# Kernel tuning notes

Hardware: AMD Instinct MI355X
Metric: run time of the kernel (lower is better)

## Reference

```python
import jax, jax.numpy as jnp
import numpy as np

N = 50000; E = 800000; B = 500; L = 42
F_IN = 35; HEADS = 10; F_H = 35; F_G = 350
VOCAB = 26; EMB = 128; NF = 16; OUT_DIM = 128; K = 8
NEG_SLOPE = 0.2


def setup_inputs() -> dict:
    key = jax.random.key(0)
    ks = jax.random.split(key, 16)
    inp = {}
    inp['x'] = jax.random.normal(ks[0], (N, F_IN), jnp.float32)
    inp['edge_index'] = jax.random.randint(ks[1], (2, E), 0, N, dtype=jnp.int32)
    inp['batch'] = jnp.sort(jax.random.randint(ks[2], (N,), 0, B, dtype=jnp.int32))
    inp['target'] = jax.random.randint(ks[3], (B, L), 0, VOCAB, dtype=jnp.int32)
    # --- learned parameters ---
    inp['W_gat'] = jax.random.normal(ks[4], (F_IN, HEADS * F_H), jnp.float32) * 0.1
    inp['att_src'] = jax.random.normal(ks[5], (HEADS, F_H), jnp.float32) * 0.1
    inp['att_dst'] = jax.random.normal(ks[6], (HEADS, F_H), jnp.float32) * 0.1
    inp['b_gat'] = jnp.zeros((HEADS * F_H,), jnp.float32)
    inp['W_gcn'] = jax.random.normal(ks[7], (F_G, F_G), jnp.float32) * 0.05
    inp['b_gcn'] = jnp.zeros((F_G,), jnp.float32)
    inp['W_fcg1'] = jax.random.normal(ks[8], (2 * F_G, 1500), jnp.float32) * 0.03
    inp['b_fcg1'] = jnp.zeros((1500,), jnp.float32)
    inp['W_fcg2'] = jax.random.normal(ks[9], (1500, OUT_DIM), jnp.float32) * 0.03
    inp['b_fcg2'] = jnp.zeros((OUT_DIM,), jnp.float32)
    inp['emb_xt'] = jax.random.normal(ks[10], (VOCAB, EMB), jnp.float32) * 0.1
    inp['W_conv'] = jax.random.normal(ks[11], (NF, EMB, K), jnp.float32) * 0.05
    inp['b_conv'] = jnp.zeros((NF,), jnp.float32)
    inp['W_fcxt'] = jax.random.normal(ks[12], (NF * 35, OUT_DIM), jnp.float32) * 0.05
    inp['b_fcxt'] = jnp.zeros((OUT_DIM,), jnp.float32)
    inp['W_fc1'] = jax.random.normal(ks[13], (256, 512), jnp.float32) * 0.05
    inp['b_fc1'] = jnp.zeros((512,), jnp.float32)
    inp['W_out'] = jax.random.normal(ks[14], (512, 1), jnp.float32) * 0.05
    inp['b_out'] = jnp.zeros((1,), jnp.float32)
    return inp


def _add_self_loops(edge_index):
    loop = jnp.arange(N, dtype=edge_index.dtype)
    src = jnp.concatenate([edge_index[0], loop])
    dst = jnp.concatenate([edge_index[1], loop])
    return src, dst


def _gat_conv(x, src, dst, W, att_src, att_dst, b):
    # h: [N, H, C]
    h = (x @ W).reshape(N, HEADS, F_H)
    a_s = jnp.einsum('nhc,hc->nh', h, att_src)  # [N, H]
    a_d = jnp.einsum('nhc,hc->nh', h, att_dst)
    e = jax.nn.leaky_relu(a_s[src] + a_d[dst], NEG_SLOPE)  # [Etot, H]
    # segment softmax over incoming edges per destination node, per head
    m = jax.ops.segment_max(e, dst, num_segments=N)
    m = jnp.where(jnp.isfinite(m), m, 0.0)
    ex = jnp.exp(e - m[dst])
    den = jax.ops.segment_sum(ex, dst, num_segments=N)
    alpha = ex / (den[dst] + 1e-16)  # [Etot, H]
    out = jax.ops.segment_sum(h[src] * alpha[:, :, None], dst, num_segments=N)
    return out.reshape(N, HEADS * F_H) + b, alpha


def _gcn_conv(x, src, dst, W, b):
    deg = jax.ops.segment_sum(jnp.ones_like(dst, jnp.float32), dst, num_segments=N)
    dinv = jnp.where(deg > 0, deg ** -0.5, 0.0)
    norm = dinv[src] * dinv[dst]  # symmetric normalization
    h = x @ W
    return jax.ops.segment_sum(h[src] * norm[:, None], dst, num_segments=N) + b


def reference(x, edge_index, batch, target, W_gat, att_src, att_dst, b_gat,
              W_gcn, b_gcn, W_fcg1, b_fcg1, W_fcg2, b_fcg2, emb_xt,
              W_conv, b_conv, W_fcxt, b_fcxt, W_fc1, b_fc1, W_out, b_out):
    src, dst = _add_self_loops(edge_index)
    # --- graph branch ---
    xg, alpha = _gat_conv(x, src, dst, W_gat, att_src, att_dst, b_gat)
    xg = jax.nn.relu(xg)
    xg = jax.nn.relu(_gcn_conv(xg, src, dst, W_gcn, b_gcn))
    # global max + mean pool per graph
    gmax = jax.ops.segment_max(xg, batch, num_segments=B)
    gsum = jax.ops.segment_sum(xg, batch, num_segments=B)
    cnt = jax.ops.segment_sum(jnp.ones((N,), jnp.float32), batch, num_segments=B)
    gmean = gsum / jnp.maximum(cnt, 1.0)[:, None]
    xg = jnp.concatenate([gmax, gmean], axis=1)  # [B, 700]
    xg = jax.nn.relu(xg @ W_fcg1 + b_fcg1)
    xg = xg @ W_fcg2 + b_fcg2  # [B, 128] (dropout is identity in eval)
    # --- protein branch ---
    emb = emb_xt[target]                      # [B, L, 128]
    emb = jnp.transpose(emb, (0, 2, 1))       # [B, 128, L]
    conv = jax.lax.conv_general_dilated(
        emb, W_conv, window_strides=(1,), padding='VALID',
        dimension_numbers=('NCH', 'OIH', 'NCH'))  # [B, 16, 35]
    conv = conv + b_conv[None, :, None]
    xt = conv.reshape(B, NF * 35)
    xt = xt @ W_fcxt + b_fcxt                 # [B, 128]
    # --- fusion ---
    xc = jnp.concatenate([xg, xt], axis=1)    # [B, 256]
    xc = jax.nn.relu(xc @ W_fc1 + b_fc1)
    out = jax.nn.sigmoid(xc @ W_out + b_out)  # [B, 1]
    return out, alpha
```

## Files before the change

### kernel.cpp

```cpp
#include <hip/hip_runtime.h>
#include <math.h>

#define NN 50000
#define EE 800000
#define BB 500
#define LL 42
#define NHEAD 10
#define FH 35
#define FG 350
#define ETOT (EE + NN)
#define NCHUNK ((NN + 511) / 512)

#define KPAD 384
#define LDH2 352
#define MPAD 50048
#define MB2  512

typedef unsigned short ushort_t;
typedef __attribute__((ext_vector_type(8))) short short8v;
typedef __attribute__((ext_vector_type(4))) float float4v;

__device__ __forceinline__ float lrelu(float x) { return x > 0.f ? x : 0.2f * x; }

__device__ __forceinline__ ushort_t f2bf(float f) {
    unsigned int u = __float_as_uint(f);
    u += 0x7fffu + ((u >> 16) & 1u);
    return (ushort_t)(u >> 16);
}
__device__ __forceinline__ float bflo(unsigned u) { return __uint_as_float(u << 16); }
__device__ __forceinline__ float bfhi(unsigned u) { return __uint_as_float(u & 0xffff0000u); }
__device__ __forceinline__ unsigned packbf(float a, float b) {
    return (unsigned)f2bf(a) | ((unsigned)f2bf(b) << 16);
}

__device__ __forceinline__ void async_cp16(const void* g, void* l) {
    __builtin_amdgcn_global_load_lds((const __attribute__((address_space(1))) unsigned int*)g,
                                     (__attribute__((address_space(3))) unsigned int*)l, 16, 0, 0);
}

__global__ __launch_bounds__(256) void k_init(int* deg, int* cur) {
    int i = blockIdx.x * 256 + threadIdx.x;
    if (i < NN) { deg[i] = 1; cur[i] = 0; }
}

__global__ __launch_bounds__(256) void k_deg(const int* __restrict__ ei, int* deg) {
    int i = blockIdx.x * 256 + threadIdx.x;
    if (i < EE) atomicAdd(&deg[ei[EE + i]], 1);
}

__global__ __launch_bounds__(512) void k_scan1(const int* __restrict__ deg, int* part) {
    int i = blockIdx.x * 512 + threadIdx.x;
    int lane = threadIdx.x & 63, wv = threadIdx.x >> 6;
    int x = (i < NN) ? deg[i] : 0;
    #pragma unroll
    for (int d = 32; d; d >>= 1) x += __shfl_xor(x, d);
    __shared__ int wsum[8];
    if (lane == 0) wsum[wv] = x;
    __syncthreads();
    if (threadIdx.x == 0) {
        int s = 0;
        #pragma unroll
        for (int w = 0; w < 8; w++) s += wsum[w];
        part[blockIdx.x] = s;
    }
}

__global__ __launch_bounds__(64) void k_scan2(const int* __restrict__ part, int* pscan) {
    int l = threadIdx.x;
    int v0 = (l < NCHUNK) ? part[l] : 0;
    #pragma unroll
    for (int d = 1; d < 64; d <<= 1) { int t = __shfl_up(v0, d); if (l >= d) v0 += t; }
    int tot0 = __shfl(v0, 63);
    int v1 = (64 + l < NCHUNK) ? part[64 + l] : 0;
    #pragma unroll
    for (int d = 1; d < 64; d <<= 1) { int t = __shfl_up(v1, d); if (l >= d) v1 += t; }
    v1 += tot0;
    if (l < NCHUNK) pscan[l] = v0;
    if (64 + l < NCHUNK) pscan[64 + l] = v1;
}

__global__ __launch_bounds__(512) void k_scan3(const int* __restrict__ deg, const int* __restrict__ pscan,
                                               int* offs) {
    int i = blockIdx.x * 512 + threadIdx.x;
    int lane = threadIdx.x & 63, wv = threadIdx.x >> 6;
    int x = (i < NN) ? deg[i] : 0;
    int incl = x;
    #pragma unroll
    for (int d = 1; d < 64; d <<= 1) { int t = __shfl_up(incl, d); if (lane >= d) incl += t; }
    __shared__ int wtot[8];
    if (lane == 63) wtot[wv] = incl;
    __syncthreads();
    int woff = 0;
    for (int w = 0; w < wv; w++) woff += wtot[w];
    int base = (blockIdx.x == 0) ? 0 : pscan[blockIdx.x - 1];
    if (i < NN) offs[i] = base + woff + incl - x;
}

__global__ __launch_bounds__(256) void k_scatter(const int* __restrict__ ei, const int* __restrict__ offs,
                                                 int* cur, int* csr_src) {
    int i = blockIdx.x * 256 + threadIdx.x;
    if (i < EE) {
        int s = ei[i], d = ei[EE + i];
        int slot = atomicAdd(&cur[d], 1);
        csr_src[offs[d] + slot] = s;
    } else if (i < ETOT) {
        int v = i - EE;
        int slot = atomicAdd(&cur[v], 1);
        csr_src[offs[v] + slot] = v;
    }
}

__global__ __launch_bounds__(256) void k_dinv(const int* __restrict__ deg, float* dinv) {
    int i = blockIdx.x * 256 + threadIdx.x;
    if (i < NN) dinv[i] = rsqrtf((float)deg[i]);
}

__global__ __launch_bounds__(256) void k_prep_att(const float* __restrict__ W_gat, const float* __restrict__ att_s,
                                                  const float* __restrict__ att_d,
                                                  float* __restrict__ wS, float* __restrict__ wD) {
    int i = blockIdx.x * 256 + threadIdx.x;
    if (i >= FG) return;
    int hd = i / 35, c = i % 35;
    float ss = 0.f, dd = 0.f;
    for (int cc = 0; cc < 35; cc++) {
        float w = W_gat[c * FG + hd * 35 + cc];
        ss += w * att_s[hd * 35 + cc];
        dd += w * att_d[hd * 35 + cc];
    }
    wS[i] = ss;
    wD[i] = dd;
}

__global__ __launch_bounds__(256) void k_prep_node(const float* __restrict__ x, const float* __restrict__ wS,
                                                   const float* __restrict__ wD, ushort_t* __restrict__ xfb,
                                                   float* __restrict__ a_s, float* __restrict__ a_d) {
    __shared__ float sw[FG], dw[FG];
    int tid = threadIdx.x;
    for (int i = tid; i < FG; i += 256) { sw[i] = wS[i]; dw[i] = wD[i]; }
    __syncthreads();
    int n = blockIdx.x * 256 + tid;
    if (n >= NN) return;
    float xr[35];
    #pragma unroll
    for (int c = 0; c < 35; c++) xr[c] = x[(size_t)n * 35 + c];
    unsigned* xo = (unsigned*)(xfb + (size_t)n * 40);
    #pragma unroll
    for (int w = 0; w < 17; w++) xo[w] = packbf(xr[2 * w], xr[2 * w + 1]);
    xo[17] = packbf(xr[34], 0.f);
    xo[18] = 0u; xo[19] = 0u;
    #pragma unroll
    for (int hd = 0; hd < NHEAD; hd++) {
        const float* ws = &sw[hd * 35];
        const float* wd = &dw[hd * 35];
        float as = 0.f, ad = 0.f;
        #pragma unroll
        for (int c = 0; c < 35; c++) { float v = xr[c]; as += v * ws[c]; ad += v * wd[c]; }
        a_s[n * NHEAD + hd] = as;
        a_d[n * NHEAD + hd] = ad;
    }
}

__global__ __launch_bounds__(256) void k_prep_wbd(const float* __restrict__ W_gat, ushort_t* __restrict__ Wt) {
    int i = blockIdx.x * 256 + threadIdx.x;
    if (i >= KPAD * KPAD) return;
    int n = i / KPAD, k = i % KPAD;
    int hd = k / 36, cc = k % 36;
    float v = 0.f;
    if (n < FG && cc < 35 && hd == n / 35) v = W_gat[cc * FG + n];
    Wt[i] = f2bf(v);
}

__global__ __launch_bounds__(256) void k_prep_wgcn(const float* __restrict__ W, ushort_t* __restrict__ Wt) {
    int i = blockIdx.x * 256 + threadIdx.x;
    if (i >= KPAD * KPAD) return;
    int n = i / KPAD, k = i % KPAD;
    float v = (n < FG && k < FG) ? W[k * FG + n] : 0.f;
    Wt[i] = f2bf(v);
}

__global__ __launch_bounds__(256) void k_prep_w(const float* __restrict__ W, ushort_t* __restrict__ Wt,
                                                int K, int N, int KP, int NP) {
    int i = blockIdx.x * 256 + threadIdx.x;
    if (i >= KP * NP) return;
    int k = i / NP, n = i % NP;
    float v = (k < K && n < N) ? W[(size_t)k * N + n] : 0.f;
    Wt[(size_t)n * KP + k] = f2bf(v);
}

__global__ __launch_bounds__(256) void k_cast_pad(const float* __restrict__ src, ushort_t* __restrict__ dst,
                                                  int M, int K, int MP, int KP) {
    int i = blockIdx.x * 256 + threadIdx.x;
    if (i >= MP * KP) return;
    int r = i / KP, k = i % KP;
    dst[i] = (r < M && k < K) ? f2bf(src[(size_t)r * K + k]) : (ushort_t)0;
}

__global__ __launch_bounds__(256) void k_zero_tail(ushort_t* buf) {
    int i = blockIdx.x * 256 + threadIdx.x;
    int total = (MPAD - NN) * KPAD;
    if (i < total) buf[(size_t)NN * KPAD + i] = 0;
}

__global__ __launch_bounds__(256) void k_mfma(const ushort_t* __restrict__ A, const ushort_t* __restrict__ Bt,
                                              void* __restrict__ C, int M, int Nv, int ldc, int lda,
                                              int ksteps, const float* __restrict__ bias, int act, int bf16out,
                                              int bdiag, int nst) {
    __shared__ ushort_t As[128 * 64];
    __shared__ ushort_t Bs[64 * 64];
    int tid = threadIdx.x;
    int wid = tid >> 6, lane = tid & 63;
    int m0 = blockIdx.y * 128, n0 = blockIdx.x * 64;
    int wm0 = (wid >> 1) * 64, wn0 = (wid & 1) * 32;
    int srow = tid >> 3;
    int scol = (tid & 7) * 8;
    float4v acc[4][2] = {{{0.f,0.f,0.f,0.f},{0.f,0.f,0.f,0.f}},
                         {{0.f,0.f,0.f,0.f},{0.f,0.f,0.f,0.f}},
                         {{0.f,0.f,0.f,0.f},{0.f,0.f,0.f,0.f}},
                         {{0.f,0.f,0.f,0.f},{0.f,0.f,0.f,0.f}}};
    int a_off = (wm0 + (lane & 15)) * 64 + (lane >> 4) * 8;
    int b_off = (wn0 + (lane & 15)) * 64 + (lane >> 4) * 8;
    int ks0 = 0, ks1 = ksteps;
    if (bdiag) {
        int hlo = n0 / 35;
        int hhi = (n0 + 63) / 35; if (hhi > 9) hhi = 9;
        ks0 = (hlo * 36) >> 6;
        ks1 = (hhi * 36 + 36 + 63) >> 6;
    }
    for (int ks = ks0; ks < ks1; ks++) {
        int k0 = ks * 64;
        #pragma unroll
        for (int r = 0; r < 4; r++) {
            const ushort_t* g = A + (size_t)(m0 + r * 32 + srow) * lda + k0 + scol;
            async_cp16(g, As + (r * 256 + tid) * 8);
        }
        #pragma unroll
        for (int r = 0; r < 2; r++) {
            const ushort_t* g = Bt + (size_t)(n0 + r * 32 + srow) * lda + k0 + scol;
            async_cp16(g, Bs + (r * 256 + tid) * 8);
        }
        __syncthreads();
        #pragma unroll
        for (int kh = 0; kh < 2; kh++) {
            short8v b0 = *(const short8v*)&Bs[b_off + kh * 32];
            short8v b1 = *(const short8v*)&Bs[b_off + 16 * 64 + kh * 32];
            #pragma unroll
            for (int mi = 0; mi < 4; mi++) {
                short8v a = *(const short8v*)&As[a_off + mi * 16 * 64 + kh * 32];
                acc[mi][0] = __builtin_amdgcn_mfma_f32_16x16x32_bf16(a, b0, acc[mi][0], 0, 0, 0);
                acc[mi][1] = __builtin_amdgcn_mfma_f32_16x16x32_bf16(a, b1, acc[mi][1], 0, 0, 0);
            }
        }
        __syncthreads();
    }
    int lm = m0 + wm0 + (lane >> 4) * 4;
    int lc = n0 + wn0 + (lane & 15);
    #pragma unroll
    for (int mi = 0; mi < 4; mi++) {
        #pragma unroll
        for (int ni = 0; ni < 2; ni++) {
            int col = lc + ni * 16;
            if (col >= nst) continue;
            float bv = (bias != nullptr && col < Nv) ? bias[col] : 0.f;
            #pragma unroll
            for (int r = 0; r < 4; r++) {
                int row = lm + mi * 16 + r;
                if (row >= M) continue;
                float v = acc[mi][ni][r] + bv;
                if (act) v = fmaxf(v, 0.f);
                if (col >= Nv) v = 0.f;
                if (bf16out) ((ushort_t*)C)[(size_t)row * ldc + col] = f2bf(v);
                else         ((float*)C)[(size_t)row * ldc + col] = v;
            }
        }
    }
}

__global__ __launch_bounds__(128) void k_gat_agg(const ushort_t* __restrict__ xfb, const float* __restrict__ a_s,
                                                 const float* __restrict__ a_d,
                                                 const int* __restrict__ csr_src,
                                                 const int* __restrict__ offs, const int* __restrict__ deg,
                                                 ushort_t* __restrict__ Zb, float* __restrict__ denArr) {
    int wid = blockIdx.x * 2 + (threadIdx.x >> 6);
    int lane = threadIdx.x & 63;
    if (wid >= NN) return;
    int o0 = offs[wid], d = deg[wid];
    bool mine = (lane < NHEAD);
    float adv = mine ? a_d[wid * NHEAD + lane] : 0.f;
    int h1 = lane / 18,          c1 = lane % 18;
    int h2 = (lane + 64) / 18,   c2 = (lane + 64) % 18;
    bool g3 = lane < 52;
    int h3 = g3 ? (lane + 128) / 18 : 0;
    int c3 = g3 ? (lane + 128) % 18 : 0;
    float den = 0.f;
    float a1l = 0.f, a1h = 0.f, a2l = 0.f, a2h = 0.f, a3l = 0.f, a3h = 0.f;
    const unsigned* x32 = (const unsigned*)xfb;
    int i = 0;
    for (; i + 4 <= d; i += 4) {
        int s0 = csr_src[o0 + i],     s1 = csr_src[o0 + i + 1];
        int s2 = csr_src[o0 + i + 2], s3 = csr_src[o0 + i + 3];
        const unsigned* x0 = x32 + (size_t)s0 * 20;
        const unsigned* x1 = x32 + (size_t)s1 * 20;
        const unsigned* x2 = x32 + (size_t)s2 * 20;
        const unsigned* x3 = x32 + (size_t)s3 * 20;
        float as0 = mine ? a_s[s0 * NHEAD + lane] : 0.f;
        float as1 = mine ? a_s[s1 * NHEAD + lane] : 0.f;
        float as2 = mine ? a_s[s2 * NHEAD + lane] : 0.f;
        float as3 = mine ? a_s[s3 * NHEAD + lane] : 0.f;
        unsigned u01 = x0[c1], u02 = x0[c2], u03 = x0[c3];
        unsigned u11 = x1[c1], u12 = x1[c2], u13 = x1[c3];
        unsigned u21 = x2[c1], u22 = x2[c2], u23 = x2[c3];
        unsigned u31 = x3[c1], u32 = x3[c2], u33 = x3[c3];
        float ex0 = __expf(lrelu(as0 + adv));
        float ex1 = __expf(lrelu(as1 + adv));
        float ex2 = __expf(lrelu(as2 + adv));
        float ex3 = __expf(lrelu(as3 + adv));
        den += (ex0 + ex1) + (ex2 + ex3);
        float e01 = __shfl(ex0, h1), e02 = __shfl(ex0, h2), e03 = __shfl(ex0, h3);
        float e11 = __shfl(ex1, h1), e12 = __shfl(ex1, h2), e13 = __shfl(ex1, h3);
        float e21 = __shfl(ex2, h1), e22 = __shfl(ex2, h2), e23 = __shfl(ex2, h3);
        float e31 = __shfl(ex3, h1), e32 = __shfl(ex3, h2), e33 = __shfl(ex3, h3);
        a1l += e01 * bflo(u01) + e11 * bflo(u11) + e21 * bflo(u21) + e31 * bflo(u31);
        a1h += e01 * bfhi(u01) + e11 * bfhi(u11) + e21 * bfhi(u21) + e31 * bfhi(u31);
        a2l += e02 * bflo(u02) + e12 * bflo(u12) + e22 * bflo(u22) + e32 * bflo(u32);
        a2h += e02 * bfhi(u02) + e12 * bfhi(u12) + e22 * bfhi(u22) + e32 * bfhi(u32);
        a3l += e03 * bflo(u03) + e13 * bflo(u13) + e23 * bflo(u23) + e33 * bflo(u33);
        a3h += e03 * bfhi(u03) + e13 * bfhi(u13) + e23 * bfhi(u23) + e33 * bfhi(u33);
    }
    for (; i < d; i++) {
        int s = csr_src[o0 + i];
        const unsigned* x0 = x32 + (size_t)s * 20;
        float as0 = mine ? a_s[s * NHEAD + lane] : 0.f;
        unsigned u01 = x0[c1], u02 = x0[c2], u03 = x0[c3];
        float ex0 = __expf(lrelu(as0 + adv));
        den += ex0;
        float e01 = __shfl(ex0, h1), e02 = __shfl(ex0, h2), e03 = __shfl(ex0, h3);
        a1l += e01 * bflo(u01);  a1h += e01 * bfhi(u01);
        a2l += e02 * bflo(u02);  a2h += e02 * bfhi(u02);
        a3l += e03 * bflo(u03);  a3h += e03 * bfhi(u03);
    }
    float rden = 1.f / (den + 1e-16f);
    if (mine) denArr[wid * NHEAD + lane] = den;
    float r1 = __shfl(rden, h1), r2 = __shfl(rden, h2), r3 = __shfl(rden, h3);
    unsigned* zr = (unsigned*)(Zb + (size_t)wid * KPAD);
    __builtin_nontemporal_store(packbf(a1l * r1, a1h * r1), &zr[lane]);
    __builtin_nontemporal_store(packbf(a2l * r2, a2h * r2), &zr[lane + 64]);
    __builtin_nontemporal_store(g3 ? packbf(a3l * r3, a3h * r3) : 0u, &zr[lane + 128]);
}

__global__ __launch_bounds__(256) void k_alpha(const int* __restrict__ ei, const float* __restrict__ a_s,
                                               const float* __restrict__ a_d, const float* __restrict__ den,
                                               float* __restrict__ alphaOut) {
    int i = blockIdx.x * 256 + threadIdx.x;
    if (i >= ETOT * NHEAD) return;
    int e = i / NHEAD, hd = i % NHEAD;
    int s, dst;
    if (e < EE) { s = ei[e]; dst = ei[EE + e]; }
    else { s = dst = e - EE; }
    float ex = __expf(lrelu(a_s[s * NHEAD + hd] + a_d[dst * NHEAD + hd]));
    __builtin_nontemporal_store(ex / (den[dst * NHEAD + hd] + 1e-16f), &alphaOut[i]);
}

__global__ __launch_bounds__(128) void k_gcn_agg(const ushort_t* __restrict__ h2b,
                                                 const int* __restrict__ csr_src,
                                                 const int* __restrict__ offs, const int* __restrict__ deg,
                                                 const float* __restrict__ dinv, const float* __restrict__ b_gcn,
                                                 ushort_t* __restrict__ xg2b) {
    int wid = blockIdx.x * 2 + (threadIdx.x >> 6);
    int lane = threadIdx.x & 63;
    if (wid >= NN) return;
    int o0 = offs[wid], d = deg[wid];
    float wv = dinv[wid];
    bool g3 = lane < 48;
    int w3 = g3 ? (lane + 128) : 0;
    float aL0 = 0.f, aH0 = 0.f, aL1 = 0.f, aH1 = 0.f, aL2 = 0.f, aH2 = 0.f;
    const unsigned* h32 = (const unsigned*)h2b;
    int i = 0;
    for (; i + 4 <= d; i += 4) {
        int s0 = csr_src[o0 + i],     s1 = csr_src[o0 + i + 1];
        int s2 = csr_src[o0 + i + 2], s3 = csr_src[o0 + i + 3];
        float q0 = dinv[s0], q1 = dinv[s1], q2 = dinv[s2], q3 = dinv[s3];
        const unsigned* h0 = h32 + (size_t)s0 * (LDH2 / 2);
        const unsigned* h1 = h32 + (size_t)s1 * (LDH2 / 2);
        const unsigned* h2 = h32 + (size_t)s2 * (LDH2 / 2);
        const unsigned* h3 = h32 + (size_t)s3 * (LDH2 / 2);
        unsigned u00 = h0[lane], u01 = h0[lane + 64], u02 = h0[w3];
        unsigned u10 = h1[lane], u11 = h1[lane + 64], u12 = h1[w3];
        unsigned u20 = h2[lane], u21 = h2[lane + 64], u22 = h2[w3];
        unsigned u30 = h3[lane], u31 = h3[lane + 64], u32 = h3[w3];
        aL0 += q0 * bflo(u00) + q1 * bflo(u10) + q2 * bflo(u20) + q3 * bflo(u30);
        aH0 += q0 * bfhi(u00) + q1 * bfhi(u10) + q2 * bfhi(u20) + q3 * bfhi(u30);
        aL1 += q0 * bflo(u01) + q1 * bflo(u11) + q2 * bflo(u21) + q3 * bflo(u31);
        aH1 += q0 * bfhi(u01) + q1 * bfhi(u11) + q2 * bfhi(u21) + q3 * bfhi(u31);
        aL2 += q0 * bflo(u02) + q1 * bflo(u12) + q2 * bflo(u22) + q3 * bflo(u32);
        aH2 += q0 * bfhi(u02) + q1 * bfhi(u12) + q2 * bfhi(u22) + q3 * bfhi(u32);
    }
    for (; i < d; i++) {
        int s = csr_src[o0 + i];
        float ws = dinv[s];
        const unsigned* hr = h32 + (size_t)s * (LDH2 / 2);
        unsigned u0 = hr[lane], u1 = hr[lane + 64], u2 = hr[w3];
        aL0 += ws * bflo(u0);  aH0 += ws * bfhi(u0);
        aL1 += ws * bflo(u1);  aH1 += ws * bfhi(u1);
        aL2 += ws * bflo(u2);  aH2 += ws * bfhi(u2);
    }
    unsigned* orow = (unsigned*)(xg2b + (size_t)wid * FG);
    {
        int f = 2 * lane;
        __builtin_nontemporal_store(packbf(fmaxf(wv * aL0 + b_gcn[f], 0.f),
                                           fmaxf(wv * aH0 + b_gcn[f + 1], 0.f)), &orow[lane]);
    }
    {
        int f = 128 + 2 * lane;
        __builtin_nontemporal_store(packbf(fmaxf(wv * aL1 + b_gcn[f], 0.f),
                                           fmaxf(wv * aH1 + b_gcn[f + 1], 0.f)), &orow[64 + lane]);
    }
    if (lane < 47) {
        int f = 256 + 2 * lane;
        __builtin_nontemporal_store(packbf(fmaxf(wv * aL2 + b_gcn[f], 0.f),
                                           fmaxf(wv * aH2 + b_gcn[f + 1], 0.f)), &orow[128 + lane]);
    }
}

__device__ __forceinline__ int lowerB(const int* a, int n, int key) {
    int lo = 0, hi = n;
    while (lo < hi) { int mid = (lo + hi) >> 1; if (a[mid] < key) lo = mid + 1; else hi = mid; }
    return lo;
}

__global__ __launch_bounds__(256) void k_pool(const ushort_t* __restrict__ xg2b, const int* __restrict__ batch,
                                              float* __restrict__ pooled) {
    int g = blockIdx.x;
    int w = threadIdx.x;
    if (w >= 175) return;
    int s = lowerB(batch, NN, g);
    int e = lowerB(batch, NN, g + 1);
    const unsigned* base = (const unsigned*)xg2b;
    float mx0 = -INFINITY, mx1 = -INFINITY, sm0 = 0.f, sm1 = 0.f;
    int n = s;
    for (; n + 2 <= e; n += 2) {
        unsigned ua = base[(size_t)n * 175 + w];
        unsigned ub = base[(size_t)(n + 1) * 175 + w];
        float a0 = bflo(ua), a1 = bfhi(ua), b0 = bflo(ub), b1 = bfhi(ub);
        mx0 = fmaxf(mx0, fmaxf(a0, b0));
        mx1 = fmaxf(mx1, fmaxf(a1, b1));
        sm0 += a0 + b0;
        sm1 += a1 + b1;
    }
    for (; n < e; n++) {
        unsigned ua = base[(size_t)n * 175 + w];
        float a0 = bflo(ua), a1 = bfhi(ua);
        mx0 = fmaxf(mx0, a0);
        mx1 = fmaxf(mx1, a1);
        sm0 += a0;
        sm1 += a1;
    }
    float rc = 1.f / fmaxf((float)(e - s), 1.f);
    pooled[g * 700 + 2 * w]       = mx0;
    pooled[g * 700 + 2 * w + 1]   = mx1;
    pooled[g * 700 + FG + 2 * w]     = sm0 * rc;
    pooled[g * 700 + FG + 2 * w + 1] = sm1 * rc;
}

__global__ __launch_bounds__(256) void k_conv(const int* __restrict__ target, const float* __restrict__ emb,
                                              const float* __restrict__ Wc, const float* __restrict__ bc,
                                              float* __restrict__ xt) {
    __shared__ float embL[26 * 132];
    __shared__ float WL[16 * 8 * 128];
    __shared__ int   tgL[2 * LL];
    int tid = threadIdx.x;
    int b0 = blockIdx.x * 2;
    for (int i = tid; i < 26 * 128; i += 256) {
        int r = i >> 7, e = i & 127;
        embL[r * 132 + e] = emb[i];
    }
    for (int i = tid; i < 16384; i += 256) {
        int f = i >> 10, rem = i & 1023, k = rem >> 7, e = rem & 127;
        WL[i] = Wc[f * 1024 + e * 8 + k];
    }
    if (tid < 2 * LL) tgL[tid] = target[b0 * LL + tid];
    __syncthreads();
    #pragma unroll
    for (int pass = 0; pass < 2; pass++) {
        int r = tid + pass * 256;
        if (r >= 280) break;
        int bl = r / 140, rem = r % 140;
        int fq = rem / 35, t = rem % 35;
        const int* tg = &tgL[bl * LL];
        float ac0 = 0.f, ac1 = 0.f, ac2 = 0.f, ac3 = 0.f;
        for (int k = 0; k < 8; k++) {
            const float* er = &embL[tg[t + k] * 132];
            const float* w0 = &WL[((fq * 4 + 0) * 8 + k) * 128];
            const float* w1 = &WL[((fq * 4 + 1) * 8 + k) * 128];
            const float* w2 = &WL[((fq * 4 + 2) * 8 + k) * 128];
            const float* w3 = &WL[((fq * 4 + 3) * 8 + k) * 128];
            #pragma unroll 8
            for (int e = 0; e < 128; e += 4) {
                float4 a = *(const float4*)&er[e];
                float4 q0 = *(const float4*)&w0[e];
                float4 q1 = *(const float4*)&w1[e];
                float4 q2 = *(const float4*)&w2[e];
                float4 q3 = *(const float4*)&w3[e];
                ac0 += a.x * q0.x + a.y * q0.y + a.z * q0.z + a.w * q0.w;
                ac1 += a.x * q1.x + a.y * q1.y + a.z * q1.z + a.w * q1.w;
                ac2 += a.x * q2.x + a.y * q2.y + a.z * q2.z + a.w * q2.w;
                ac3 += a.x * q3.x + a.y * q3.y + a.z * q3.z + a.w * q3.w;
            }
        }
        int b = b0 + bl, fb = fq * 4;
        xt[b * 560 + (fb + 0) * 35 + t] = ac0 + bc[fb + 0];
        xt[b * 560 + (fb + 1) * 35 + t] = ac1 + bc[fb + 1];
        xt[b * 560 + (fb + 2) * 35 + t] = ac2 + bc[fb + 2];
        xt[b * 560 + (fb + 3) * 35 + t] = ac3 + bc[fb + 3];
    }
}

__global__ __launch_bounds__(256) void k_out(const float* __restrict__ f1, const float* __restrict__ W_out,
                                             const float* __restrict__ b_out, float* __restrict__ out) {
    int wid = (blockIdx.x * blockDim.x + threadIdx.x) >> 6;
    int lane = threadIdx.x & 63;
    if (wid >= BB) return;
    const float* xr = f1 + (size_t)wid * 512;
    float acc = 0.f;
    #pragma unroll
    for (int k = 0; k < 8; k++) acc += xr[lane + k * 64] * W_out[lane + k * 64];
    #pragma unroll
    for (int d = 32; d; d >>= 1) acc += __shfl_xor(acc, d);
    if (lane == 0) out[wid] = 1.f / (1.f + __expf(-(acc + b_out[0])));
}

extern "C" void kernel_launch(void* const* d_in, const int* in_sizes, int n_in,
                              void* d_out, int out_size, void* d_ws, size_t ws_size,
                              hipStream_t stream) {
    const float* x      = (const float*)d_in[0];
    const int*   ei     = (const int*)d_in[1];
    const int*   batch  = (const int*)d_in[2];
    const int*   target = (const int*)d_in[3];
    const float* W_gat  = (const float*)d_in[4];
    const float* att_s  = (const float*)d_in[5];
    const float* att_d  = (const float*)d_in[6];
    const float* b_gat  = (const float*)d_in[7];
    const float* W_gcn  = (const float*)d_in[8];
    const float* b_gcn  = (const float*)d_in[9];
    const float* W_fcg1 = (const float*)d_in[10];
    const float* b_fcg1 = (const float*)d_in[11];
    const float* W_fcg2 = (const float*)d_in[12];
    const float* b_fcg2 = (const float*)d_in[13];
    const float* embxt  = (const float*)d_in[14];
    const float* W_conv = (const float*)d_in[15];
    const float* b_conv = (const float*)d_in[16];
    const float* W_fcxt = (const float*)d_in[17];
    const float* b_fcxt = (const float*)d_in[18];
    const float* W_fc1  = (const float*)d_in[19];
    const float* b_fc1  = (const float*)d_in[20];
    const float* W_out  = (const float*)d_in[21];
    const float* b_out  = (const float*)d_in[22];

    float* out_sig  = (float*)d_out;
    float* alphaOut = (float*)d_out + BB;

    size_t o = 0;
    auto alloc = [&](size_t bytes) -> void* {
        o = (o + 255) & ~(size_t)255;
        void* p = (char*)d_ws + o;
        o += bytes;
        return p;
    };
    int*   deg     = (int*)alloc((size_t)NN * 4);
    int*   cur     = (int*)alloc((size_t)NN * 4);
    int*   offs    = (int*)alloc((size_t)NN * 4);
    int*   part    = (int*)alloc(128 * 4);
    int*   pscan   = (int*)alloc(128 * 4);
    int*   csr_src = (int*)alloc((size_t)ETOT * 4);
    float* dinv    = (float*)alloc((size_t)NN * 4);
    float* a_s     = (float*)alloc((size_t)NN * NHEAD * 4);
    float* a_d     = (float*)alloc((size_t)NN * NHEAD * 4);
    float* denArr  = (float*)alloc((size_t)NN * NHEAD * 4);
    ushort_t* xfb  = (ushort_t*)alloc((size_t)NN * 40 * 2);
    float* wS      = (float*)alloc((size_t)FG * 4);
    float* wD      = (float*)alloc((size_t)FG * 4);
    ushort_t* WtBD = (ushort_t*)alloc((size_t)KPAD * KPAD * 2);
    ushort_t* WtGC = (ushort_t*)alloc((size_t)KPAD * KPAD * 2);
    ushort_t* WtF1 = (ushort_t*)alloc((size_t)1536 * 704 * 2);
    ushort_t* WtF2 = (ushort_t*)alloc((size_t)128 * 1536 * 2);
    ushort_t* WtFX = (ushort_t*)alloc((size_t)128 * 576 * 2);
    ushort_t* WtFC = (ushort_t*)alloc((size_t)512 * 256 * 2);
    float* pooled  = (float*)alloc((size_t)BB * 700 * 4);
    ushort_t* pooledb = (ushort_t*)alloc((size_t)MB2 * 704 * 2);
    ushort_t* t1b  = (ushort_t*)alloc((size_t)MB2 * 1536 * 2);
    float* xt      = (float*)alloc((size_t)BB * 560 * 4);
    ushort_t* xtb  = (ushort_t*)alloc((size_t)MB2 * 576 * 2);
    ushort_t* xcb  = (ushort_t*)alloc((size_t)MB2 * 256 * 2);
    float* f1      = (float*)alloc((size_t)MB2 * 512 * 4);
    ushort_t* hb   = (ushort_t*)alloc((size_t)MPAD * KPAD * 2);
    char*  R2      = (char*)alloc((size_t)NN * FG * 4);
    ushort_t* xg1b = (ushort_t*)R2;
    ushort_t* xg2b = (ushort_t*)R2;
    (void)ws_size; (void)n_in; (void)in_sizes; (void)out_size;

    auto mfma = [&](const ushort_t* A, const ushort_t* Bt, void* C, const float* bias,
                    int M2, int Nv, int NP, int ldc, int KP, int act, int bf16out, int bdiag, int nst) {
        dim3 g(NP / 64, M2 / 128);
        k_mfma<<<g, 256, 0, stream>>>(A, Bt, C, M2, Nv, ldc, KP, KP / 64, bias, act, bf16out, bdiag, nst);
    };

    k_init<<<(NN + 255) / 256, 256, 0, stream>>>(deg, cur);
    k_deg<<<(EE + 255) / 256, 256, 0, stream>>>(ei, deg);
    k_scan1<<<NCHUNK, 512, 0, stream>>>(deg, part);
    k_scan2<<<1, 64, 0, stream>>>(part, pscan);
    k_scan3<<<NCHUNK, 512, 0, stream>>>(deg, pscan, offs);
    k_scatter<<<(ETOT + 255) / 256, 256, 0, stream>>>(ei, offs, cur, csr_src);
    k_dinv<<<(NN + 255) / 256, 256, 0, stream>>>(deg, dinv);

    k_prep_att<<<2, 256, 0, stream>>>(W_gat, att_s, att_d, wS, wD);
    k_prep_node<<<(NN + 255) / 256, 256, 0, stream>>>(x, wS, wD, xfb, a_s, a_d);
    k_prep_wbd<<<(KPAD * KPAD + 255) / 256, 256, 0, stream>>>(W_gat, WtBD);
    k_prep_wgcn<<<(KPAD * KPAD + 255) / 256, 256, 0, stream>>>(W_gcn, WtGC);
    k_prep_w<<<(704 * 1536 + 255) / 256, 256, 0, stream>>>(W_fcg1, WtF1, 700, 1500, 704, 1536);
    k_prep_w<<<(1536 * 128 + 255) / 256, 256, 0, stream>>>(W_fcg2, WtF2, 1500, 128, 1536, 128);
    k_prep_w<<<(576 * 128 + 255) / 256, 256, 0, stream>>>(W_fcxt, WtFX, 560, 128, 576, 128);
    k_prep_w<<<(256 * 512 + 255) / 256, 256, 0, stream>>>(W_fc1, WtFC, 256, 512, 256, 512);
    k_zero_tail<<<((MPAD - NN) * KPAD + 255) / 256, 256, 0, stream>>>(hb);

    k_gat_agg<<<(NN + 1) / 2, 128, 0, stream>>>(xfb, a_s, a_d, csr_src, offs, deg, hb, denArr);
    k_alpha<<<(ETOT * NHEAD + 255) / 256, 256, 0, stream>>>(ei, a_s, a_d, denArr, alphaOut);
    mfma(hb, WtBD, xg1b, b_gat, MPAD, FG, KPAD, KPAD, KPAD, 1, 1, 1, KPAD);

    mfma(xg1b, WtGC, hb, nullptr, MPAD, FG, KPAD, LDH2, KPAD, 0, 1, 0, LDH2);
    k_gcn_agg<<<(NN + 1) / 2, 128, 0, stream>>>(hb, csr_src, offs, deg, dinv, b_gcn, xg2b);

    k_pool<<<BB, 256, 0, stream>>>(xg2b, batch, pooled);
    k_cast_pad<<<(MB2 * 704 + 255) / 256, 256, 0, stream>>>(pooled, pooledb, BB, 700, MB2, 704);
    mfma(pooledb, WtF1, t1b, b_fcg1, MB2, 1500, 1536, 1536, 704, 1, 1, 0, 1536);
    mfma(t1b, WtF2, xcb, b_fcg2, MB2, 128, 128, 256, 1536, 0, 1, 0, 128);
    k_conv<<<250, 256, 0, stream>>>(target, embxt, W_conv, b_conv, xt);
    k_cast_pad<<<(MB2 * 576 + 255) / 256, 256, 0, stream>>>(xt, xtb, BB, 560, MB2, 576);
    mfma(xtb, WtFX, xcb + 128, b_fcxt, MB2, 128, 128, 256, 576, 0, 1, 0, 128);
    mfma(xcb, WtFC, f1, b_fc1, MB2, 512, 512, 512, 256, 1, 0, 0, 512);
    k_out<<<(BB + 3) / 4, 256, 0, stream>>>(f1, W_out, b_out, out_sig);
}
```

Measured before the change: 582.9 us.

## Pack bf16 source attention into node records and fuse small prep kernels

Stores the per-node source attention logits as bf16 inside the same 96-byte node record as the bf16 features, so the GAT aggregation gathers both with one cacheline instead of a separate a_s read. The dinv computation moves into the scan kernel, the six weight-prep launches merge into one kernel, and the tail zeroing of the hidden buffer moves into the aggregation kernel, which cuts launch count. k_alpha rounds a_s to bf16 so alpha stays consistent with the aggregation. The cost is lower precision for the attention logits.

```diff
diff --git a/kernel.cpp b/kernel.cpp
--- a/kernel.cpp
+++ b/kernel.cpp
@@ -15,6 +15,7 @@
 #define LDH2 352
 #define MPAD 50048
 #define MB2  512
+#define NDW  24
 
 typedef unsigned short ushort_t;
 typedef __attribute__((ext_vector_type(8))) short short8v;
@@ -29,6 +30,7 @@
 }
 __device__ __forceinline__ float bflo(unsigned u) { return __uint_as_float(u << 16); }
 __device__ __forceinline__ float bfhi(unsigned u) { return __uint_as_float(u & 0xffff0000u); }
+__device__ __forceinline__ float bfu(ushort_t u) { return __uint_as_float(((unsigned)u) << 16); }
 __device__ __forceinline__ unsigned packbf(float a, float b) {
     return (unsigned)f2bf(a) | ((unsigned)f2bf(b) << 16);
 }
@@ -80,7 +82,7 @@
 }
 
 __global__ __launch_bounds__(512) void k_scan3(const int* __restrict__ deg, const int* __restrict__ pscan,
-                                               int* offs) {
+                                               int* offs, float* dinv) {
     int i = blockIdx.x * 512 + threadIdx.x;
     int lane = threadIdx.x & 63, wv = threadIdx.x >> 6;
     int x = (i < NN) ? deg[i] : 0;
@@ -93,7 +95,10 @@
     int woff = 0;
     for (int w = 0; w < wv; w++) woff += wtot[w];
     int base = (blockIdx.x == 0) ? 0 : pscan[blockIdx.x - 1];
-    if (i < NN) offs[i] = base + woff + incl - x;
+    if (i < NN) {
+        offs[i] = base + woff + incl - x;
+        dinv[i] = rsqrtf((float)x);
+    }
 }
 
 __global__ __launch_bounds__(256) void k_scatter(const int* __restrict__ ei, const int* __restrict__ offs,
@@ -110,11 +115,6 @@
     }
 }
 
-__global__ __launch_bounds__(256) void k_dinv(const int* __restrict__ deg, float* dinv) {
-    int i = blockIdx.x * 256 + threadIdx.x;
-    if (i < NN) dinv[i] = rsqrtf((float)deg[i]);
-}
-
 __global__ __launch_bounds__(256) void k_prep_att(const float* __restrict__ W_gat, const float* __restrict__ att_s,
                                                   const float* __restrict__ att_d,
                                                   float* __restrict__ wS, float* __restrict__ wD) {
@@ -132,7 +132,7 @@
 }
 
 __global__ __launch_bounds__(256) void k_prep_node(const float* __restrict__ x, const float* __restrict__ wS,
-                                                   const float* __restrict__ wD, ushort_t* __restrict__ xfb,
+                                                   const float* __restrict__ wD, ushort_t* __restrict__ nd,
                                                    float* __restrict__ a_s, float* __restrict__ a_d) {
     __shared__ float sw[FG], dw[FG];
     int tid = threadIdx.x;
@@ -143,11 +143,11 @@
     float xr[35];
     #pragma unroll
     for (int c = 0; c < 35; c++) xr[c] = x[(size_t)n * 35 + c];
-    unsigned* xo = (unsigned*)(xfb + (size_t)n * 40);
+    unsigned* xo = (unsigned*)(nd + (size_t)n * (2 * NDW));
     #pragma unroll
     for (int w = 0; w < 17; w++) xo[w] = packbf(xr[2 * w], xr[2 * w + 1]);
     xo[17] = packbf(xr[34], 0.f);
-    xo[18] = 0u; xo[19] = 0u;
+    float asv[NHEAD];
     #pragma unroll
     for (int hd = 0; hd < NHEAD; hd++) {
         const float* ws = &sw[hd * 35];
@@ -155,37 +155,66 @@
         float as = 0.f, ad = 0.f;
         #pragma unroll
         for (int c = 0; c < 35; c++) { float v = xr[c]; as += v * ws[c]; ad += v * wd[c]; }
+        asv[hd] = as;
         a_s[n * NHEAD + hd] = as;
         a_d[n * NHEAD + hd] = ad;
     }
-}
-
-__global__ __launch_bounds__(256) void k_prep_wbd(const float* __restrict__ W_gat, ushort_t* __restrict__ Wt) {
+    #pragma unroll
+    for (int j = 0; j < 5; j++) xo[18 + j] = packbf(asv[2 * j], asv[2 * j + 1]);
+    xo[23] = 0u;
+}
+
+__global__ __launch_bounds__(256) void k_prep_weights(
+    const float* __restrict__ Wg, const float* __restrict__ Wc,
+    const float* __restrict__ W1, const float* __restrict__ W2,
+    const float* __restrict__ WX, const float* __restrict__ WF,
+    ushort_t* __restrict__ BD, ushort_t* __restrict__ GC,
+    ushort_t* __restrict__ F1, ushort_t* __restrict__ F2,
+    ushort_t* __restrict__ FX, ushort_t* __restrict__ FC) {
     int i = blockIdx.x * 256 + threadIdx.x;
-    if (i >= KPAD * KPAD) return;
-    int n = i / KPAD, k = i % KPAD;
-    int hd = k / 36, cc = k % 36;
-    float v = 0.f;
-    if (n < FG && cc < 35 && hd == n / 35) v = W_gat[cc * FG + n];
-    Wt[i] = f2bf(v);
-}
-
-__global__ __launch_bounds__(256) void k_prep_wgcn(const float* __restrict__ W, ushort_t* __restrict__ Wt) {
-    int i = blockIdx.x * 256 + threadIdx.x;
-    if (i >= KPAD * KPAD) return;
-    int n = i / KPAD, k = i % KPAD;
-    float v = (n < FG && k < FG) ? W[k * FG + n] : 0.f;
-    Wt[i] = f2bf(v);
-}
-
-__global__ __launch_bounds__(256) void k_prep_w(const float* __restrict__ W, ushort_t* __restrict__ Wt,
-                                                int K, int N, int KP, int NP) {
-    int i = blockIdx.x * 256 + threadIdx.x;
-    if (i >= KP * NP) return;
-    int k = i / NP, n = i % NP;
-    float v = (k < K && n < N) ? W[(size_t)k * N + n] : 0.f;
-    Wt[(size_t)n * KP + k] = f2bf(v);
-}
+    if (i < KPAD * KPAD) {
+        int n = i / KPAD, k = i % KPAD;
+        int hd = k / 36, cc = k % 36;
+        float v = 0.f;
+        if (n < FG && cc < 35 && hd == n / 35) v = Wg[cc * FG + n];
+        BD[i] = f2bf(v);
+        return;
+    }
+    i -= KPAD * KPAD;
+    if (i < KPAD * KPAD) {
+        int n = i / KPAD, k = i % KPAD;
+        float v = (n < FG && k < FG) ? Wc[k * FG + n] : 0.f;
+        GC[i] = f2bf(v);
+        return;
+    }
+    i -= KPAD * KPAD;
+    if (i < 704 * 1536) {
+        int k = i / 1536, n = i % 1536;
+        float v = (k < 700 && n < 1500) ? W1[(size_t)k * 1500 + n] : 0.f;
+        F1[(size_t)n * 704 + k] = f2bf(v);
+        return;
+    }
+    i -= 704 * 1536;
+    if (i < 1536 * 128) {
+        int k = i / 128, n = i % 128;
+        float v = (k < 1500) ? W2[(size_t)k * 128 + n] : 0.f;
+        F2[(size_t)n * 1536 + k] = f2bf(v);
+        return;
+    }
+    i -= 1536 * 128;
+    if (i < 576 * 128) {
+        int k = i / 128, n = i % 128;
+        float v = (k < 560) ? WX[(size_t)k * 128 + n] : 0.f;
+        FX[(size_t)n * 576 + k] = f2bf(v);
+        return;
+    }
+    i -= 576 * 128;
+    if (i < 256 * 512) {
+        int k = i / 512, n = i % 512;
+        FC[(size_t)n * 256 + k] = f2bf(WF[(size_t)k * 512 + n]);
+    }
+}
+#define PREPW_TOTAL (KPAD * KPAD * 2 + 704 * 1536 + 1536 * 128 + 576 * 128 + 256 * 512)
 
 __global__ __launch_bounds__(256) void k_cast_pad(const float* __restrict__ src, ushort_t* __restrict__ dst,
                                                   int M, int K, int MP, int KP) {
@@ -193,12 +222,6 @@
     if (i >= MP * KP) return;
     int r = i / KP, k = i % KP;
     dst[i] = (r < M && k < K) ? f2bf(src[(size_t)r * K + k]) : (ushort_t)0;
-}
-
-__global__ __launch_bounds__(256) void k_zero_tail(ushort_t* buf) {
-    int i = blockIdx.x * 256 + threadIdx.x;
-    int total = (MPAD - NN) * KPAD;
-    if (i < total) buf[(size_t)NN * KPAD + i] = 0;
 }
 
 __global__ __launch_bounds__(256) void k_mfma(const ushort_t* __restrict__ A, const ushort_t* __restrict__ Bt,
@@ -275,14 +298,21 @@
     }
 }
 
-__global__ __launch_bounds__(128) void k_gat_agg(const ushort_t* __restrict__ xfb, const float* __restrict__ a_s,
+__global__ __launch_bounds__(128) void k_gat_agg(const ushort_t* __restrict__ nd,
                                                  const float* __restrict__ a_d,
                                                  const int* __restrict__ csr_src,
                                                  const int* __restrict__ offs, const int* __restrict__ deg,
                                                  ushort_t* __restrict__ Zb, float* __restrict__ denArr) {
     int wid = blockIdx.x * 2 + (threadIdx.x >> 6);
     int lane = threadIdx.x & 63;
-    if (wid >= NN) return;
+    if (wid >= MPAD) return;
+    unsigned* zr = (unsigned*)(Zb + (size_t)wid * KPAD);
+    if (wid >= NN) {
+        __builtin_nontemporal_store(0u, &zr[lane]);
+        __builtin_nontemporal_store(0u, &zr[lane + 64]);
+        __builtin_nontemporal_store(0u, &zr[lane + 128]);
+        return;
+    }
     int o0 = offs[wid], d = deg[wid];
     bool mine = (lane < NHEAD);
     float adv = mine ? a_d[wid * NHEAD + lane] : 0.f;
@@ -293,19 +323,19 @@
     int c3 = g3 ? (lane + 128) % 18 : 0;
     float den = 0.f;
     float a1l = 0.f, a1h = 0.f, a2l = 0.f, a2h = 0.f, a3l = 0.f, a3h = 0.f;
-    const unsigned* x32 = (const unsigned*)xfb;
+    const unsigned* x32 = (const unsigned*)nd;
     int i = 0;
     for (; i + 4 <= d; i += 4) {
         int s0 = csr_src[o0 + i],     s1 = csr_src[o0 + i + 1];
         int s2 = csr_src[o0 + i + 2], s3 = csr_src[o0 + i + 3];
-        const unsigned* x0 = x32 + (size_t)s0 * 20;
-        const unsigned* x1 = x32 + (size_t)s1 * 20;
-        const unsigned* x2 = x32 + (size_t)s2 * 20;
-        const unsigned* x3 = x32 + (size_t)s3 * 20;
-        float as0 = mine ? a_s[s0 * NHEAD + lane] : 0.f;
-        float as1 = mine ? a_s[s1 * NHEAD + lane] : 0.f;
-        float as2 = mine ? a_s[s2 * NHEAD + lane] : 0.f;
-        float as3 = mine ? a_s[s3 * NHEAD + lane] : 0.f;
+        const unsigned* x0 = x32 + (size_t)s0 * NDW;
+        const unsigned* x1 = x32 + (size_t)s1 * NDW;
+        const unsigned* x2 = x32 + (size_t)s2 * NDW;
+        const unsigned* x3 = x32 + (size_t)s3 * NDW;
+        float as0 = mine ? bfu(((const ushort_t*)x0)[36 + lane]) : 0.f;
+        float as1 = mine ? bfu(((const ushort_t*)x1)[36 + lane]) : 0.f;
+        float as2 = mine ? bfu(((const ushort_t*)x2)[36 + lane]) : 0.f;
+        float as3 = mine ? bfu(((const ushort_t*)x3)[36 + lane]) : 0.f;
         unsigned u01 = x0[c1], u02 = x0[c2], u03 = x0[c3];
         unsigned u11 = x1[c1], u12 = x1[c2], u13 = x1[c3];
         unsigned u21 = x2[c1], u22 = x2[c2], u23 = x2[c3];
@@ -328,8 +358,8 @@
     }
     for (; i < d; i++) {
         int s = csr_src[o0 + i];
-        const unsigned* x0 = x32 + (size_t)s * 20;
-        float as0 = mine ? a_s[s * NHEAD + lane] : 0.f;
+        const unsigned* x0 = x32 + (size_t)s * NDW;
+        float as0 = mine ? bfu(((const ushort_t*)x0)[36 + lane]) : 0.f;
         unsigned u01 = x0[c1], u02 = x0[c2], u03 = x0[c3];
         float ex0 = __expf(lrelu(as0 + adv));
         den += ex0;
@@ -341,7 +371,6 @@
     float rden = 1.f / (den + 1e-16f);
     if (mine) denArr[wid * NHEAD + lane] = den;
     float r1 = __shfl(rden, h1), r2 = __shfl(rden, h2), r3 = __shfl(rden, h3);
-    unsigned* zr = (unsigned*)(Zb + (size_t)wid * KPAD);
     __builtin_nontemporal_store(packbf(a1l * r1, a1h * r1), &zr[lane]);
     __builtin_nontemporal_store(packbf(a2l * r2, a2h * r2), &zr[lane + 64]);
     __builtin_nontemporal_store(g3 ? packbf(a3l * r3, a3h * r3) : 0u, &zr[lane + 128]);
@@ -356,7 +385,8 @@
     int s, dst;
     if (e < EE) { s = ei[e]; dst = ei[EE + e]; }
     else { s = dst = e - EE; }
-    float ex = __expf(lrelu(a_s[s * NHEAD + hd] + a_d[dst * NHEAD + hd]));
+    float zs = bfu(f2bf(a_s[s * NHEAD + hd]));
+    float ex = __expf(lrelu(zs + a_d[dst * NHEAD + hd]));
     __builtin_nontemporal_store(ex / (den[dst * NHEAD + hd] + 1e-16f), &alphaOut[i]);
 }
 
@@ -575,7 +605,7 @@
     float* a_s     = (float*)alloc((size_t)NN * NHEAD * 4);
     float* a_d     = (float*)alloc((size_t)NN * NHEAD * 4);
     float* denArr  = (float*)alloc((size_t)NN * NHEAD * 4);
-    ushort_t* xfb  = (ushort_t*)alloc((size_t)NN * 40 * 2);
+    ushort_t* nd   = (ushort_t*)alloc((size_t)NN * 48 * 2);
     float* wS      = (float*)alloc((size_t)FG * 4);
     float* wD      = (float*)alloc((size_t)FG * 4);
     ushort_t* WtBD = (ushort_t*)alloc((size_t)KPAD * KPAD * 2);
@@ -607,21 +637,16 @@
     k_deg<<<(EE + 255) / 256, 256, 0, stream>>>(ei, deg);
     k_scan1<<<NCHUNK, 512, 0, stream>>>(deg, part);
     k_scan2<<<1, 64, 0, stream>>>(part, pscan);
-    k_scan3<<<NCHUNK, 512, 0, stream>>>(deg, pscan, offs);
+    k_scan3<<<NCHUNK, 512, 0, stream>>>(deg, pscan, offs, dinv);
     k_scatter<<<(ETOT + 255) / 256, 256, 0, stream>>>(ei, offs, cur, csr_src);
-    k_dinv<<<(NN + 255) / 256, 256, 0, stream>>>(deg, dinv);
 
     k_prep_att<<<2, 256, 0, stream>>>(W_gat, att_s, att_d, wS, wD);
-    k_prep_node<<<(NN + 255) / 256, 256, 0, stream>>>(x, wS, wD, xfb, a_s, a_d);
-    k_prep_wbd<<<(KPAD * KPAD + 255) / 256, 256, 0, stream>>>(W_gat, WtBD);
-    k_prep_wgcn<<<(KPAD * KPAD + 255) / 256, 256, 0, stream>>>(W_gcn, WtGC);
-    k_prep_w<<<(704 * 1536 + 255) / 256, 256, 0, stream>>>(W_fcg1, WtF1, 700, 1500, 704, 1536);
-    k_prep_w<<<(1536 * 128 + 255) / 256, 256, 0, stream>>>(W_fcg2, WtF2, 1500, 128, 1536, 128);
-    k_prep_w<<<(576 * 128 + 255) / 256, 256, 0, stream>>>(W_fcxt, WtFX, 560, 128, 576, 128);
-    k_prep_w<<<(256 * 512 + 255) / 256, 256, 0, stream>>>(W_fc1, WtFC, 256, 512, 256, 512);
-    k_zero_tail<<<((MPAD - NN) * KPAD + 255) / 256, 256, 0, stream>>>(hb);
-
-    k_gat_agg<<<(NN + 1) / 2, 128, 0, stream>>>(xfb, a_s, a_d, csr_src, offs, deg, hb, denArr);
+    k_prep_node<<<(NN + 255) / 256, 256, 0, stream>>>(x, wS, wD, nd, a_s, a_d);
+    k_prep_weights<<<(PREPW_TOTAL + 255) / 256, 256, 0, stream>>>(W_gat, W_gcn, W_fcg1, W_fcg2,
+                                                                  W_fcxt, W_fc1,
+                                                                  WtBD, WtGC, WtF1, WtF2, WtFX, WtFC);
+
+    k_gat_agg<<<MPAD / 2, 128, 0, stream>>>(nd, a_d, csr_src, offs, deg, hb, denArr);
     k_alpha<<<(ETOT * NHEAD + 255) / 256, 256, 0, stream>>>(ei, a_s, a_d, denArr, alphaOut);
     mfma(hb, WtBD, xg1b, b_gat, MPAD, FG, KPAD, KPAD, KPAD, 1, 1, 1, KPAD);
 
```

Result: no change. 576.0 us (-1.2%).
